# Kernel tuning notes

Measured on AMD Instinct MI355X. Metric: run time of the kernel, lower is better.

Reference implementation:

```python
import jax, jax.numpy as jnp
import numpy as np

EMBED_DIM = 2048
NUM_HEADS = 32
NUM_KV_HEADS = 8
HEAD_DIM = EMBED_DIM // NUM_HEADS  # 64
KV_DIM = HEAD_DIM * NUM_KV_HEADS   # 512
ROPE_BASE = 10000.0


def rope_cos_sin(seq_len, dim):
    inv_freq = 1.0 / (ROPE_BASE ** (jnp.arange(0, dim, 2, dtype=jnp.float32) / dim))
    t = jnp.arange(seq_len, dtype=jnp.float32)
    freqs = jnp.outer(t, inv_freq)                 # [T, dim/2]
    emb = jnp.concatenate([freqs, freqs], axis=-1)  # [T, dim]
    return jnp.cos(emb), jnp.sin(emb)


def rotate_half(x):
    half = x.shape[-1] // 2
    return jnp.concatenate([-x[..., half:], x[..., :half]], axis=-1)


def setup_inputs() -> dict:
    key = jax.random.key(0)
    k_x, k_q, k_k, k_v, k_o = jax.random.split(key, 5)
    B, T, C = 2, 2048, EMBED_DIM
    s = 1.0 / np.sqrt(C)
    x = jax.random.normal(k_x, (B, T, C), dtype=jnp.float32)
    # Linear weights stored as [in, out]; no bias (bias=False)
    Wq = jax.random.normal(k_q, (C, EMBED_DIM), dtype=jnp.float32) * s
    Wk = jax.random.normal(k_k, (C, KV_DIM), dtype=jnp.float32) * s
    Wv = jax.random.normal(k_v, (C, KV_DIM), dtype=jnp.float32) * s
    Wo = jax.random.normal(k_o, (C, EMBED_DIM), dtype=jnp.float32) * s
    return {"x": x, "Wq": Wq, "Wk": Wk, "Wv": Wv, "Wo": Wo}


def reference(x, Wq, Wk, Wv, Wo):
    B, T, C = x.shape
    H, KVH, D = NUM_HEADS, NUM_KV_HEADS, HEAD_DIM
    scale = D ** -0.5
    rep = H // KVH

    q = (x @ Wq).reshape(B, T, H, D).transpose(0, 2, 1, 3)    # [B,H,T,D]
    k = (x @ Wk).reshape(B, T, KVH, D).transpose(0, 2, 1, 3)  # [B,KVH,T,D]
    v = (x @ Wv).reshape(B, T, KVH, D).transpose(0, 2, 1, 3)
    # repeat_interleave over head dim to expand KV heads
    k = jnp.repeat(k, rep, axis=1)  # [B,H,T,D]
    v = jnp.repeat(v, rep, axis=1)

    cos, sin = rope_cos_sin(T, D)
    cos = cos[None, None, :, :]
    sin = sin[None, None, :, :]
    q = q * cos + rotate_half(q) * sin
    k = k * cos + rotate_half(k) * sin

    att = jnp.einsum('bhtd,bhsd->bhts', q, k) * scale  # [B,H,T,T]
    att = jax.nn.softmax(att, axis=-1)                 # mask=None, dropout eval
    y = jnp.einsum('bhts,bhsd->bhtd', att, v)          # [B,H,T,D]
    y = y.transpose(0, 2, 1, 3).reshape(B, T, C)
    return y @ Wo
```

## Files before the change

### kernel.cpp

```cpp
#include <hip/hip_runtime.h>
#include <stdint.h>

#define Tn   2048
#define Cn   2048
#define Hn   32
#define KVHn 8
#define Dn   64
#define MR   4096
#define NQKV 3072
#define KD   2048

typedef __attribute__((ext_vector_type(4))) float fx4;
typedef __attribute__((ext_vector_type(8))) short frag8;

#define MFMA(a,b,c) __builtin_amdgcn_mfma_f32_16x16x32_bf16((a),(b),(c),0,0,0)

struct __align__(16) U16x8 { unsigned short s[8]; };

__device__ __forceinline__ unsigned short f2bf(float x){
  union { float f; unsigned u; } v; v.f = x;
  return (unsigned short)((v.u + 0x7FFFu + ((v.u >> 16) & 1u)) >> 16);
}
__device__ __forceinline__ float bf2f(unsigned short h){
  union { unsigned u; float f; } v; v.u = ((unsigned)h) << 16; return v.f;
}
__device__ __forceinline__ float sexp2(float x){
#if __has_builtin(__builtin_amdgcn_exp2f)
  return __builtin_amdgcn_exp2f(x);
#else
  return exp2f(x);
#endif
}
__device__ __forceinline__ unsigned cvtpk(float a, float b){
  unsigned r; asm("v_cvt_pk_bf16_f32 %0, %1, %2" : "=v"(r) : "v"(a), "v"(b)); return r;
}

typedef const __attribute__((address_space(1))) void cas1_void;
typedef __attribute__((address_space(3))) void as3_void;
__device__ __forceinline__ void gld16(const void* g, void* l){
  __builtin_amdgcn_global_load_lds((cas1_void*)g, (as3_void*)l, 16, 0, 0);
}

__global__ __launch_bounds__(256) void k_prep(const float* __restrict__ x, unsigned short* __restrict__ xb,
                                              const float* __restrict__ Wq, const float* __restrict__ Wk,
                                              const float* __restrict__ Wv, unsigned short* __restrict__ wqkvt,
                                              const float* __restrict__ Wo, unsigned short* __restrict__ wot,
                                              float2* __restrict__ cs){
  __shared__ float tile[64][65];
  int blk = blockIdx.x, t = threadIdx.x;
  if (blk < 2048) {
    size_t blockbase = (size_t)blk * 4096;
    #pragma unroll
    for (int j = 0; j < 4; ++j) {
      size_t i = blockbase + j * 1024 + t * 4;
      float4 v = *(const float4*)(x + i);
      ushort4 o; o.x = f2bf(v.x); o.y = f2bf(v.y); o.z = f2bf(v.z); o.w = f2bf(v.w);
      *(ushort4*)(xb + i) = o;
    }
    return;
  }
  if (blk >= 4608) {
    int i = (blk - 4608) * 256 + t;
    int tp = i >> 5, d = i & 31;
    float inv = powf(10000.0f, -(float)d * (1.0f/32.0f));
    float fr = (float)tp * inv;
    cs[i] = make_float2(cosf(fr), sinf(fr));
    return;
  }
  const float* src; int col0, ld, n0, k0; unsigned short* outp;
  if (blk < 3584) {
    int bx = blk - 2048; n0 = (bx % 48) * 64; k0 = (bx / 48) * 64; outp = wqkvt;
    if (n0 < 2048)      { src = Wq; col0 = n0;        ld = 2048; }
    else if (n0 < 2560) { src = Wk; col0 = n0 - 2048; ld = 512;  }
    else                { src = Wv; col0 = n0 - 2560; ld = 512;  }
  } else {
    int bx = blk - 3584; n0 = (bx % 32) * 64; k0 = (bx / 32) * 64; outp = wot;
    src = Wo; col0 = n0; ld = 2048;
  }
  int r = t >> 2, cc = (t & 3) << 4;
  const float* p = src + (size_t)(k0 + r) * ld + col0 + cc;
  #pragma unroll
  for (int j = 0; j < 16; j += 4) {
    float4 v = *(const float4*)(p + j);
    tile[r][cc + j + 0] = v.x; tile[r][cc + j + 1] = v.y;
    tile[r][cc + j + 2] = v.z; tile[r][cc + j + 3] = v.w;
  }
  __syncthreads();
  int n = t >> 2, kc = (t & 3) << 4;
  unsigned short* q = outp + (size_t)(n0 + n) * 2048 + k0 + kc;
  U16x8 o0, o1;
  #pragma unroll
  for (int j = 0; j < 8; ++j) o0.s[j] = f2bf(tile[kc + j][n]);
  #pragma unroll
  for (int j = 0; j < 8; ++j) o1.s[j] = f2bf(tile[kc + 8 + j][n]);
  *(U16x8*)(q) = o0;
  *(U16x8*)(q + 8) = o1;
}

template<int MODE>
__global__ __launch_bounds__(256) void k_gemm(const unsigned short* __restrict__ A,
                                              const unsigned short* __restrict__ Bt,
                                              void* __restrict__ Cp,
                                              int M, int N, int K,
                                              const float2* __restrict__ cs){
  __shared__ unsigned short As[128 * 64];
  __shared__ unsigned short Bs[128 * 64];
  int tid = threadIdx.x;
  int m0 = blockIdx.y * 128, n0 = blockIdx.x * 128;
  int w = tid >> 6, ln = tid & 63, lr = ln & 15, lg = ln >> 4;
  int wm = (w >> 1) * 64, wn = (w & 1) * 64;
  fx4 acc[4][4];
  #pragma unroll
  for (int i = 0; i < 4; ++i)
    #pragma unroll
    for (int j = 0; j < 4; ++j) acc[i][j] = (fx4){0.f,0.f,0.f,0.f};
  int steps = K >> 6;
  for (int kt = 0; kt < steps; ++kt) {
    int kb = kt << 6;
    #pragma unroll
    for (int it = 0; it < 4; ++it) {
      int nch = it * 256 + tid;
      int r = nch >> 3, c = (nch & 7) ^ (r & 7);
      gld16(A  + (size_t)(m0 + r) * K + kb + c * 8, (char*)As + nch * 16);
      gld16(Bt + (size_t)(n0 + r) * K + kb + c * 8, (char*)Bs + nch * 16);
    }
    __syncthreads();
    frag8 aF[4][2], bF[4][2];
    #pragma unroll
    for (int i = 0; i < 4; ++i) {
      int ra = wm + i * 16 + lr;
      int rb = wn + i * 16 + lr;
      #pragma unroll
      for (int kk = 0; kk < 2; ++kk) {
        aF[i][kk] = *(const frag8*)((const char*)As + ra * 128 + (((lg + 4*kk) ^ (ra & 7)) << 4));
        bF[i][kk] = *(const frag8*)((const char*)Bs + rb * 128 + (((lg + 4*kk) ^ (rb & 7)) << 4));
      }
    }
    #pragma unroll
    for (int kk = 0; kk < 2; ++kk)
      #pragma unroll
      for (int i = 0; i < 4; ++i)
        #pragma unroll
        for (int j = 0; j < 4; ++j)
          acc[i][j] = MFMA(aF[i][kk], bF[j][kk], acc[i][j]);
    __syncthreads();
  }
  if (MODE == 0) {
    #pragma unroll
    for (int i = 0; i < 4; ++i) {
      int row = m0 + wm + i * 16 + lg * 4;
      #pragma unroll
      for (int j = 0; j < 4; ++j) {
        int col = n0 + wn + j * 16 + lr;
        #pragma unroll
        for (int rr = 0; rr < 4; ++rr)
          ((float*)Cp)[(size_t)(row + rr) * N + col] = acc[i][j][rr];
      }
    }
  } else {
    int nb = n0 + wn;
    unsigned short* outp = (unsigned short*)Cp;
    if (nb < 2560) {
      float sc = (n0 < 2048) ? 0.180336880f : 1.0f;
      #pragma unroll
      for (int i = 0; i < 4; ++i) {
        int rowb = m0 + wm + i * 16 + lg * 4;
        #pragma unroll
        for (int jp = 0; jp < 2; ++jp) {
          int dA = jp * 16 + lr;
          #pragma unroll
          for (int rr = 0; rr < 4; ++rr) {
            int row = rowb + rr;
            float2 cv = cs[((row & (Tn-1)) << 5) + dA];
            float a = acc[i][jp][rr], b = acc[i][jp + 2][rr];
            outp[(size_t)row * N + nb + dA]      = f2bf((a * cv.x - b * cv.y) * sc);
            outp[(size_t)row * N + nb + dA + 32] = f2bf((b * cv.x + a * cv.y) * sc);
          }
        }
      }
    } else {
      #pragma unroll
      for (int i = 0; i < 4; ++i) {
        int row = m0 + wm + i * 16 + lg * 4;
        #pragma unroll
        for (int j = 0; j < 4; ++j) {
          int col = nb + j * 16 + lr;
          #pragma unroll
          for (int rr = 0; rr < 4; ++rr)
            outp[(size_t)(row + rr) * N + col] = f2bf(acc[i][j][rr]);
        }
      }
    }
  }
}

__global__ __launch_bounds__(256) void k_vt(const unsigned short* __restrict__ qkv,
                                            unsigned short* __restrict__ vt){
  __shared__ unsigned short tl[64][66];
  int head = blockIdx.y;
  int b = head >> 3, kvh = head & 7;
  int t0 = blockIdx.x * 64;
  int t = threadIdx.x;
  int r = t >> 2, cc = (t & 3) << 4;
  const unsigned short* p = qkv + (size_t)(b * Tn + t0 + r) * NQKV + 2560 + kvh * 64 + cc;
  U16x8 v0 = *(const U16x8*)(p);
  U16x8 v1 = *(const U16x8*)(p + 8);
  #pragma unroll
  for (int j = 0; j < 8; ++j) { tl[r][cc + j] = v0.s[j]; tl[r][cc + 8 + j] = v1.s[j]; }
  __syncthreads();
  int d = t >> 2, cpair = t & 3;
  unsigned short* q = vt + ((size_t)head * 64 + d) * Tn + t0;
  #pragma unroll
  for (int ci = 0; ci < 2; ++ci) {
    int c = cpair * 2 + ci;
    U16x8 oo;
    #pragma unroll
    for (int e = 0; e < 8; ++e)
      oo.s[e] = tl[32 * (c >> 2) + 16 * (e >> 2) + 4 * (c & 3) + (e & 3)][d];
    *(U16x8*)(q + c * 8) = oo;
  }
}

__global__ __launch_bounds__(256) void k_attn(const unsigned short* __restrict__ qkv,
                                              const unsigned short* __restrict__ vt,
                                              unsigned short* __restrict__ y){
  __shared__ unsigned short Ks[2][64 * 64];
  __shared__ unsigned short Vs[2][64 * 64];
  int tid = threadIdx.x, w = tid >> 6, ln = tid & 63, lq = ln & 15, lg = ln >> 4;
  int bh = blockIdx.y, b = bh >> 5, h = bh & 31, kvh = h >> 2;
  int q0 = blockIdx.x * 128;
  frag8 qF[2][2];
  #pragma unroll
  for (int s = 0; s < 2; ++s) {
    const unsigned short* qrow = qkv + (size_t)(b * Tn + q0 + w * 32 + 16 * s + lq) * NQKV + h * 64;
    qF[s][0] = *(const frag8*)(qrow + lg * 8);
    qF[s][1] = *(const frag8*)(qrow + 32 + lg * 8);
  }
  fx4 zero4 = (fx4){0.f, 0.f, 0.f, 0.f};
  asm volatile("" : "+v"(zero4));
  int n0 = tid, n1 = 256 + tid;
  int r0 = n0 >> 3, c0 = (n0 & 7) ^ (r0 & 7);
  int r1 = n1 >> 3, c1 = (n1 & 7) ^ (r1 & 7);
  const unsigned short* kp0 = qkv + (size_t)b * Tn * NQKV + 2048 + kvh * 64 + (size_t)r0 * NQKV + c0 * 8;
  const unsigned short* kp1 = qkv + (size_t)b * Tn * NQKV + 2048 + kvh * 64 + (size_t)r1 * NQKV + c1 * 8;
  const unsigned short* vp0 = vt + ((size_t)(b * 8 + kvh) * 64 + r0) * Tn + c0 * 8;
  const unsigned short* vp1 = vt + ((size_t)(b * 8 + kvh) * 64 + r1) * Tn + c1 * 8;
  int koff0 = lq * 128 + (((lg)     ^ (lq & 7)) << 4);
  int koff1 = lq * 128 + (((lg + 4) ^ (lq & 7)) << 4);

#define STAGE(BUF) do {                                      \
    gld16(kp0, (char*)&Ks[BUF][0] + n0 * 16);                \
    gld16(kp1, (char*)&Ks[BUF][0] + n1 * 16);                \
    gld16(vp0, (char*)&Vs[BUF][0] + n0 * 16);                \
    gld16(vp1, (char*)&Vs[BUF][0] + n1 * 16);                \
    kp0 += 64 * NQKV; kp1 += 64 * NQKV; vp0 += 64; vp1 += 64;\
  } while (0)

#define PB(S, KK) ({ union { unsigned u[4]; frag8 f; } t_;                        \
    t_.u[0] = pu[S][2*(KK)][0]; t_.u[1] = pu[S][2*(KK)][1];                       \
    t_.u[2] = pu[S][2*(KK)+1][0]; t_.u[3] = pu[S][2*(KK)+1][1]; t_.f; })

#define COMPUTE(BUF) do {                                                         \
    const char* kb_ = (const char*)&Ks[BUF][0];                                   \
    const char* vb_ = (const char*)&Vs[BUF][0];                                   \
    frag8 kf[4][2];                                                               \
    _Pragma("unroll")                                                             \
    for (int mf = 0; mf < 4; ++mf) {                                              \
      kf[mf][0] = *(const frag8*)(kb_ + mf * 2048 + koff0);                       \
      kf[mf][1] = *(const frag8*)(kb_ + mf * 2048 + koff1);                       \
    }                                                                             \
    fx4 sf[2][4];                                                                 \
    __builtin_amdgcn_s_setprio(1);                                                \
    _Pragma("unroll")                                                             \
    for (int s = 0; s < 2; ++s)                                                   \
      _Pragma("unroll")                                                           \
      for (int mf = 0; mf < 4; ++mf) {                                            \
        sf[s][mf] = MFMA(kf[mf][0], qF[s][0], zero4);                             \
        sf[s][mf] = MFMA(kf[mf][1], qF[s][1], sf[s][mf]);                         \
      }                                                                           \
    __builtin_amdgcn_s_setprio(0);                                                \
    unsigned pu[2][4][2];                                                         \
    _Pragma("unroll")                                                             \
    for (int s = 0; s < 2; ++s) {                                                 \
      float ps = 0.f;                                                             \
      _Pragma("unroll")                                                           \
      for (int mf = 0; mf < 4; ++mf) {                                            \
        float p0 = sexp2(sf[s][mf][0]);                                           \
        float p1 = sexp2(sf[s][mf][1]);                                           \
        float p2 = sexp2(sf[s][mf][2]);                                           \
        float p3 = sexp2(sf[s][mf][3]);                                           \
        ps += (p0 + p1) + (p2 + p3);                                              \
        pu[s][mf][0] = cvtpk(p0, p1);                                             \
        pu[s][mf][1] = cvtpk(p2, p3);                                             \
      }                                                                           \
      lpart[s] += ps;                                                             \
    }                                                                             \
    frag8 vf[4][2];                                                               \
    _Pragma("unroll")                                                             \
    for (int df = 0; df < 4; ++df) {                                              \
      vf[df][0] = *(const frag8*)(vb_ + df * 2048 + koff0);                       \
      vf[df][1] = *(const frag8*)(vb_ + df * 2048 + koff1);                       \
    }                                                                             \
    __builtin_amdgcn_s_setprio(1);                                                \
    _Pragma("unroll")                                                             \
    for (int s = 0; s < 2; ++s)                                                   \
      _Pragma("unroll")                                                           \
      for (int df = 0; df < 4; ++df) {                                            \
        o[s][df] = MFMA(vf[df][0], PB(s, 0), o[s][df]);                           \
        o[s][df] = MFMA(vf[df][1], PB(s, 1), o[s][df]);                           \
      }                                                                           \
    __builtin_amdgcn_s_setprio(0);                                                \
  } while (0)

  fx4 o[2][4];
  float lpart[2] = {0.f, 0.f};
  #pragma unroll
  for (int s = 0; s < 2; ++s)
    #pragma unroll
    for (int i = 0; i < 4; ++i) o[s][i] = (fx4){0.f, 0.f, 0.f, 0.f};

  STAGE(0);
  __syncthreads();
  for (int kt = 0; kt < 32; kt += 2) {
    STAGE(1);
    COMPUTE(0);
    __syncthreads();
    if (kt + 2 < 32) STAGE(0);
    COMPUTE(1);
    __syncthreads();
  }
#undef STAGE
#undef COMPUTE
#undef PB

  #pragma unroll
  for (int s = 0; s < 2; ++s) {
    lpart[s] += __shfl_xor(lpart[s], 16);
    lpart[s] += __shfl_xor(lpart[s], 32);
    float inv = 1.0f / lpart[s];
    unsigned short* yp = y + (size_t)(b * Tn + q0 + w * 32 + 16 * s + lq) * Cn + h * 64;
    #pragma unroll
    for (int df = 0; df < 4; ++df) {
      unsigned lo = cvtpk(o[s][df][0] * inv, o[s][df][1] * inv);
      unsigned hi = cvtpk(o[s][df][2] * inv, o[s][df][3] * inv);
      *(uint2*)(yp + df * 16 + lg * 4) = make_uint2(lo, hi);
    }
  }
}

extern "C" void kernel_launch(void* const* d_in, const int* in_sizes, int n_in,
                              void* d_out, int out_size, void* d_ws, size_t ws_size,
                              hipStream_t stream){
  const float* x  = (const float*)d_in[0];
  const float* Wq = (const float*)d_in[1];
  const float* Wk = (const float*)d_in[2];
  const float* Wv = (const float*)d_in[3];
  const float* Wo = (const float*)d_in[4];
  char* ws = (char*)d_ws;
  size_t off = 0;
  unsigned short* xb    = (unsigned short*)(ws + off); off += (size_t)MR * KD * 2;
  unsigned short* wqkvt = (unsigned short*)(ws + off); off += (size_t)NQKV * KD * 2;
  unsigned short* wot   = (unsigned short*)(ws + off); off += (size_t)KD * KD * 2;
  unsigned short* qkv   = (unsigned short*)(ws + off); off += (size_t)MR * NQKV * 2;
  unsigned short* vtb   = (unsigned short*)(ws + off); off += (size_t)16 * 64 * Tn * 2;
  float2* cstab = (float2*)(ws + off); off += (size_t)Tn * 32 * 8;
  unsigned short* yb = xb;

  k_prep<<<4864, 256, 0, stream>>>(x, xb, Wq, Wk, Wv, wqkvt, Wo, wot, cstab);
  k_gemm<2><<<dim3(NQKV / 128, MR / 128), 256, 0, stream>>>(xb, wqkvt, qkv, MR, NQKV, KD, cstab);
  k_vt<<<dim3(Tn / 64, 16), 256, 0, stream>>>(qkv, vtb);
  k_attn<<<dim3(Tn / 128, 64), 256, 0, stream>>>(qkv, vtb, yb);
  k_gemm<0><<<dim3(KD / 128, MR / 128), 256, 0, stream>>>(yb, wot, d_out, MR, KD, KD, nullptr);
}
```

Before: 214.1 us.

## Software-pipeline attention PV MFMAs one tile behind QK MFMAs

Restructures the attention inner loop so each tile first issues the P·V MFMAs for the previous tile, then the QK^T MFMAs for the current tile, then loads V fragments and computes exp/packing for the current tile. The goal is to overlap the softmax exponentials and LDS reads with independent MFMA work instead of serialising QK → exp → PV. The first PV step runs on zero-initialised fragments and one extra PV step drains after the loop. Carrying pu and vf across iterations adds register pressure, which could cut occupancy or cause spills.

```diff
diff --git a/kernel.cpp b/kernel.cpp
--- a/kernel.cpp
+++ b/kernel.cpp
@@ -260,7 +260,17 @@
     t_.u[0] = pu[S][2*(KK)][0]; t_.u[1] = pu[S][2*(KK)][1];                       \
     t_.u[2] = pu[S][2*(KK)+1][0]; t_.u[3] = pu[S][2*(KK)+1][1]; t_.f; })
 
-#define COMPUTE(BUF) do {                                                         \
+#define PVSTEP do {                                                               \
+    _Pragma("unroll")                                                             \
+    for (int s = 0; s < 2; ++s)                                                   \
+      _Pragma("unroll")                                                           \
+      for (int df = 0; df < 4; ++df) {                                            \
+        o[s][df] = MFMA(vf[df][0], PB(s, 0), o[s][df]);                           \
+        o[s][df] = MFMA(vf[df][1], PB(s, 1), o[s][df]);                           \
+      }                                                                           \
+  } while (0)
+
+#define TILE(BUF) do {                                                            \
     const char* kb_ = (const char*)&Ks[BUF][0];                                   \
     const char* vb_ = (const char*)&Vs[BUF][0];                                   \
     frag8 kf[4][2];                                                               \
@@ -269,8 +279,9 @@
       kf[mf][0] = *(const frag8*)(kb_ + mf * 2048 + koff0);                       \
       kf[mf][1] = *(const frag8*)(kb_ + mf * 2048 + koff1);                       \
     }                                                                             \
+    __builtin_amdgcn_s_setprio(1);                                                \
+    PVSTEP;                               \
     fx4 sf[2][4];                                                                 \
-    __builtin_amdgcn_s_setprio(1);                                                \
     _Pragma("unroll")                                                             \
     for (int s = 0; s < 2; ++s)                                                   \
       _Pragma("unroll")                                                           \
@@ -279,8 +290,12 @@
         sf[s][mf] = MFMA(kf[mf][1], qF[s][1], sf[s][mf]);                         \
       }                                                                           \
     __builtin_amdgcn_s_setprio(0);                                                \
-    unsigned pu[2][4][2];                                                         \
-    _Pragma("unroll")                                                             \
+    _Pragma("unroll")              \
+    for (int df = 0; df < 4; ++df) {                                              \
+      vf[df][0] = *(const frag8*)(vb_ + df * 2048 + koff0);                       \
+      vf[df][1] = *(const frag8*)(vb_ + df * 2048 + koff1);                       \
+    }                                                                             \
+    _Pragma("unroll")                                \
     for (int s = 0; s < 2; ++s) {                                                 \
       float ps = 0.f;                                                             \
       _Pragma("unroll")                                                           \
@@ -295,42 +310,41 @@
       }                                                                           \
       lpart[s] += ps;                                                             \
     }                                                                             \
-    frag8 vf[4][2];                                                               \
-    _Pragma("unroll")                                                             \
-    for (int df = 0; df < 4; ++df) {                                              \
-      vf[df][0] = *(const frag8*)(vb_ + df * 2048 + koff0);                       \
-      vf[df][1] = *(const frag8*)(vb_ + df * 2048 + koff1);                       \
-    }                                                                             \
-    __builtin_amdgcn_s_setprio(1);                                                \
-    _Pragma("unroll")                                                             \
-    for (int s = 0; s < 2; ++s)                                                   \
-      _Pragma("unroll")                                                           \
-      for (int df = 0; df < 4; ++df) {                                            \
-        o[s][df] = MFMA(vf[df][0], PB(s, 0), o[s][df]);                           \
-        o[s][df] = MFMA(vf[df][1], PB(s, 1), o[s][df]);                           \
-      }                                                                           \
-    __builtin_amdgcn_s_setprio(0);                                                \
   } while (0)
 
   fx4 o[2][4];
   float lpart[2] = {0.f, 0.f};
-  #pragma unroll
-  for (int s = 0; s < 2; ++s)
+  unsigned pu[2][4][2];
+  frag8 vf[4][2];
+  #pragma unroll
+  for (int s = 0; s < 2; ++s) {
     #pragma unroll
     for (int i = 0; i < 4; ++i) o[s][i] = (fx4){0.f, 0.f, 0.f, 0.f};
+    #pragma unroll
+    for (int mf = 0; mf < 4; ++mf) { pu[s][mf][0] = 0u; pu[s][mf][1] = 0u; }
+  }
+  #pragma unroll
+  for (int df = 0; df < 4; ++df) {
+    vf[df][0] = (frag8){0,0,0,0,0,0,0,0};
+    vf[df][1] = (frag8){0,0,0,0,0,0,0,0};
+  }
 
   STAGE(0);
   __syncthreads();
   for (int kt = 0; kt < 32; kt += 2) {
     STAGE(1);
-    COMPUTE(0);
+    TILE(0);
     __syncthreads();
     if (kt + 2 < 32) STAGE(0);
-    COMPUTE(1);
+    TILE(1);
     __syncthreads();
   }
+  __builtin_amdgcn_s_setprio(1);
+  PVSTEP;
+  __builtin_amdgcn_s_setprio(0);
 #undef STAGE
-#undef COMPUTE
+#undef TILE
+#undef PVSTEP
 #undef PB
 
   #pragma unroll
```

Result: faster. 208.4 us (-2.7%).
